# Kernel tuning notes

Measured on AMD Instinct MI355X. Metric: run time of the kernel, lower is better.

## Reference

```python
import jax, jax.numpy as jnp
import numpy as np

NUM_HEADS = 16
HEAD_DIM = 64


def setup_inputs() -> dict:
    key = jax.random.key(0)
    k1, k2, k3 = jax.random.split(key, 3)
    B, N, D = 4, 2048, NUM_HEADS * HEAD_DIM
    q = jax.random.normal(k1, (B, N, D), dtype=jnp.float32)
    k = jax.random.normal(k2, (B, N, D), dtype=jnp.float32)
    v = jax.random.normal(k3, (B, N, D), dtype=jnp.float32)
    # causal mask: True where attention is allowed
    attn_mask = jnp.tril(jnp.ones((N, N), dtype=bool))
    return {"q": q, "k": k, "v": v, "attn_mask": attn_mask}


def reference(q, k, v, attn_mask):
    B, N, D = q.shape
    H, Hd = NUM_HEADS, HEAD_DIM
    # [B, N, H*Hd] -> [B, H, N, Hd]
    qh = q.reshape(B, N, H, Hd).transpose(0, 2, 1, 3)
    kh = k.reshape(B, N, H, Hd).transpose(0, 2, 1, 3)
    vh = v.reshape(B, N, H, Hd).transpose(0, 2, 1, 3)
    scale = 1.0 / jnp.sqrt(jnp.asarray(Hd, dtype=q.dtype))
    scores = jnp.einsum('bhqd,bhkd->bhqk', qh, kh) * scale  # [B,H,N,N]
    scores = jnp.where(attn_mask[None, None, :, :], scores, -jnp.inf)
    probs = jax.nn.softmax(scores, axis=-1)
    y = jnp.einsum('bhqk,bhkd->bhqd', probs, vh)  # [B,H,N,Hd]
    return y.transpose(0, 2, 1, 3).reshape(B, N, H * Hd)
```

## Files before the change

### kernel.cpp

```cpp
#include <hip/hip_runtime.h>

#define RS 1024
#define SEQLEN 2048

typedef __fp16 f16;
typedef __attribute__((ext_vector_type(2))) __fp16 half2v;
typedef __attribute__((ext_vector_type(4))) __fp16 half4v;
typedef __attribute__((ext_vector_type(8))) __fp16 half8v;
typedef __attribute__((ext_vector_type(4))) float float4v;

__device__ __forceinline__ half8v pack8h(float4v a, float4v b) {
  union { half8v v; half2v h[4]; } u;
  u.h[0] = __builtin_amdgcn_cvt_pkrtz(a[0], a[1]);
  u.h[1] = __builtin_amdgcn_cvt_pkrtz(a[2], a[3]);
  u.h[2] = __builtin_amdgcn_cvt_pkrtz(b[0], b[1]);
  u.h[3] = __builtin_amdgcn_cvt_pkrtz(b[2], b[3]);
  return u.v;
}

template<bool DOMASK>
__device__ __forceinline__ void compute_tile(
    const f16* __restrict__ Klds, const f16* __restrict__ VB,
    const half8v (&aq)[2], float4v (&o)[4], float& lp,
    int quad, int lm, int wlm)
{
  float4v sfr[4];
  #pragma unroll
  for (int nb = 0; nb < 4; ++nb) sfr[nb] = (float4v){0.f, 0.f, 0.f, 0.f};

  __builtin_amdgcn_s_setprio(1);
  #pragma unroll
  for (int nb = 0; nb < 4; ++nb) {
    const int row = nb*16 + lm;
    #pragma unroll
    for (int s = 0; s < 2; ++s) {
      const half8v ak = *(const half8v*)&Klds[row*64 + (((s*4 + quad) ^ (lm & 7)) * 8)];
      sfr[nb] = __builtin_amdgcn_mfma_f32_16x16x32_f16(ak, aq[s], sfr[nb], 0, 0, 0);
    }
  }
  __builtin_amdgcn_s_setprio(0);

  half4v pa[4];
  float acc = 0.f;
  #pragma unroll
  for (int nb = 0; nb < 4; ++nb) {
    float p[4];
    #pragma unroll
    for (int r = 0; r < 4; ++r) {
      const int n = nb*16 + quad*4 + r;
      const float e = __builtin_amdgcn_exp2f(sfr[nb][r]);
      p[r] = (DOMASK && (n > wlm)) ? 0.f : e;
    }
    acc += (p[0] + p[1]) + (p[2] + p[3]);
    union { half4v v; half2v h[2]; } u;
    u.h[0] = __builtin_amdgcn_cvt_pkrtz(p[0], p[1]);
    u.h[1] = __builtin_amdgcn_cvt_pkrtz(p[2], p[3]);
    pa[nb] = u.v;
  }
  lp += acc;

  __builtin_amdgcn_s_setprio(1);
  #pragma unroll
  for (int nb = 0; nb < 4; ++nb) {
    const int kvq = nb*4 + quad;
    #pragma unroll
    for (int db = 0; db < 4; ++db) {
      const half4v vb = *(const half4v*)&VB[kvq*256 + (((db*16 + lm) ^ quad) * 4)];
      o[db] = __builtin_amdgcn_mfma_f32_16x16x16f16(pa[nb], vb, o[db], 0, 0, 0);
    }
  }
  __builtin_amdgcn_s_setprio(0);
}

__global__ __launch_bounds__(256, 4) void fa_fwd(
    const float* __restrict__ Qg, const float* __restrict__ Kg,
    const float* __restrict__ Vg, float* __restrict__ Og)
{
  __shared__ __align__(16) f16 Klds[2][64*64];
  __shared__ __align__(16) f16 VB[2][64*64];

  const int tid  = threadIdx.x;
  const int w    = tid >> 6;
  const int lane = tid & 63;
  const int quad = lane >> 4;
  const int lm   = lane & 15;
  const int wlm  = w*16 + lm;

  const int bid = blockIdx.x;
  const int bh  = bid & 63;
  const int t   = 31 - (bid >> 6);

  const size_t headoff = (size_t)(bh >> 4) * SEQLEN * RS + (size_t)(bh & 15) * 64;
  const float* Kb = Kg + headoff;
  const float* Vb = Vg + headoff;

  const float qs = 0.18033688011112042f;
  half8v aq[2];
  {
    const float* qp = Qg + headoff + (size_t)(t*64 + w*16 + lm) * RS + quad*8;
    aq[0] = pack8h(*(const float4v*)qp * qs,        *(const float4v*)(qp + 4) * qs);
    aq[1] = pack8h(*(const float4v*)(qp + 32) * qs, *(const float4v*)(qp + 36) * qs);
  }

  float4v o[4] = {};
  float lp = 0.f;

  const int krow = tid >> 3, kcb = tid & 7;
  const int rgrp = tid >> 4, dgrp = tid & 15;
  const int r3 = rgrp & 3;

  float4v pk[4], pv[4];
  auto loadKV = [&](int kv0) {
    const float* kp = Kb + (size_t)(kv0 + krow) * RS + kcb*8;
    pk[0] = *(const float4v*)kp;       pk[1] = *(const float4v*)(kp + 4);
    const float* kp2 = kp + (size_t)32 * RS;
    pk[2] = *(const float4v*)kp2;      pk[3] = *(const float4v*)(kp2 + 4);
    const float* vp = Vb + (size_t)(kv0 + rgrp*4) * RS + dgrp*4;
    pv[0] = *(const float4v*)vp;
    pv[1] = *(const float4v*)(vp + RS);
    pv[2] = *(const float4v*)(vp + 2*RS);
    pv[3] = *(const float4v*)(vp + 3*RS);
  };
  auto stageKV = [&](f16* Kd, f16* Vd) {
    *(half8v*)&Kd[krow*64 + ((kcb ^ (krow & 7)) * 8)] = pack8h(pk[0], pk[1]);
    const int row2 = krow + 32;
    *(half8v*)&Kd[row2*64 + ((kcb ^ (row2 & 7)) * 8)] = pack8h(pk[2], pk[3]);
    union { half8v v8[2]; half2v h[8]; } u;
    #pragma unroll
    for (int cp = 0; cp < 4; ++cp) {
      const int c = cp ^ r3;
      u.h[cp*2]     = __builtin_amdgcn_cvt_pkrtz(pv[0][c], pv[1][c]);
      u.h[cp*2 + 1] = __builtin_amdgcn_cvt_pkrtz(pv[2][c], pv[3][c]);
    }
    f16* dst = &Vd[rgrp*256 + dgrp*16];
    *(half8v*)dst       = u.v8[0];
    *(half8v*)(dst + 8) = u.v8[1];
  };

  loadKV(0);
  stageKV(Klds[0], VB[0]);
  if (t > 0) loadKV(64);
  __syncthreads();

  for (int j = 0; j <= t; ++j) {
    const int cur = j & 1;
    if (j < t) {
      stageKV(Klds[cur ^ 1], VB[cur ^ 1]);
      if (j + 1 < t) loadKV((j + 2) * 64);
    }
    if (j < t)
      compute_tile<false>(Klds[cur], VB[cur], aq, o, lp, quad, lm, wlm);
    else
      compute_tile<true >(Klds[cur], VB[cur], aq, o, lp, quad, lm, wlm);
    __syncthreads();
  }

  float l = lp;
  l += __shfl_xor(l, 16);
  l += __shfl_xor(l, 32);
  const float linv = 1.0f / l;
  #pragma unroll
  for (int r = 0; r < 4; ++r) {
    const float nrm = __shfl(linv, quad*4 + r);
    float* op = Og + headoff + (size_t)(t*64 + w*16 + quad*4 + r) * RS;
    #pragma unroll
    for (int db = 0; db < 4; ++db)
      op[db*16 + lm] = o[db][r] * nrm;
  }
}

extern "C" void kernel_launch(void* const* d_in, const int* in_sizes, int n_in,
                              void* d_out, int out_size, void* d_ws, size_t ws_size,
                              hipStream_t stream) {
  const float* q = (const float*)d_in[0];
  const float* k = (const float*)d_in[1];
  const float* v = (const float*)d_in[2];
  float* out = (float*)d_out;
  fa_fwd<<<dim3(32 * 64), dim3(256), 0, stream>>>(q, k, v, out);
}
```

Baseline: 200.4 us.

## Process 128 query rows per block with 8 waves sharing K/V tiles

Each block now covers 128 query rows with 512 threads (8 waves), so every K/V tile loaded into shared memory serves twice as many query rows and global K/V traffic is halved. The load work is split so the upper 256 threads fetch K and the lower 256 fetch V, which halves per-thread prefetch registers. The waves covering the first 64 rows skip the final diagonal tile while the other waves compute it, which leaves some waves idle on the last iteration. The grid shrinks from 2048 to 1024 blocks, reducing the number of blocks available to spread across CUs.

Result: faster. 181.4 us (-9.5%).

```diff
diff --git a/kernel.cpp b/kernel.cpp
--- a/kernel.cpp
+++ b/kernel.cpp
@@ -72,7 +72,7 @@
   __builtin_amdgcn_s_setprio(0);
 }
 
-__global__ __launch_bounds__(256, 4) void fa_fwd(
+__global__ __launch_bounds__(512, 4) void fa_fwd(
     const float* __restrict__ Qg, const float* __restrict__ Kg,
     const float* __restrict__ Vg, float* __restrict__ Og)
 {
@@ -84,11 +84,13 @@
   const int lane = tid & 63;
   const int quad = lane >> 4;
   const int lm   = lane & 15;
-  const int wlm  = w*16 + lm;
+  const int wlm  = (w & 3)*16 + lm;
 
   const int bid = blockIdx.x;
   const int bh  = bid & 63;
-  const int t   = 31 - (bid >> 6);
+  const int st  = 15 - (bid >> 6);
+  const int j1  = 2*st + 1;
+  const int j1w = 2*st + (w >> 2);
 
   const size_t headoff = (size_t)(bh >> 4) * SEQLEN * RS + (size_t)(bh & 15) * 64;
   const float* Kb = Kg + headoff;
@@ -97,7 +99,7 @@
   const float qs = 0.18033688011112042f;
   half8v aq[2];
   {
-    const float* qp = Qg + headoff + (size_t)(t*64 + w*16 + lm) * RS + quad*8;
+    const float* qp = Qg + headoff + (size_t)(st*128 + w*16 + lm) * RS + quad*8;
     aq[0] = pack8h(*(const float4v*)qp * qs,        *(const float4v*)(qp + 4) * qs);
     aq[1] = pack8h(*(const float4v*)(qp + 32) * qs, *(const float4v*)(qp + 36) * qs);
   }
@@ -105,53 +107,63 @@
   float4v o[4] = {};
   float lp = 0.f;
 
-  const int krow = tid >> 3, kcb = tid & 7;
-  const int rgrp = tid >> 4, dgrp = tid & 15;
+  const bool doK = (tid >= 256);
+  const int kr   = tid & 255;
+  const int krow = kr >> 3, kcb = kr & 7;
+  const int rgrp = kr >> 4, dgrp = kr & 15;
   const int r3 = rgrp & 3;
 
-  float4v pk[4], pv[4];
+  float4v pr[4];
   auto loadKV = [&](int kv0) {
-    const float* kp = Kb + (size_t)(kv0 + krow) * RS + kcb*8;
-    pk[0] = *(const float4v*)kp;       pk[1] = *(const float4v*)(kp + 4);
-    const float* kp2 = kp + (size_t)32 * RS;
-    pk[2] = *(const float4v*)kp2;      pk[3] = *(const float4v*)(kp2 + 4);
-    const float* vp = Vb + (size_t)(kv0 + rgrp*4) * RS + dgrp*4;
-    pv[0] = *(const float4v*)vp;
-    pv[1] = *(const float4v*)(vp + RS);
-    pv[2] = *(const float4v*)(vp + 2*RS);
-    pv[3] = *(const float4v*)(vp + 3*RS);
+    if (doK) {
+      const float* kp = Kb + (size_t)(kv0 + krow) * RS + kcb*8;
+      pr[0] = *(const float4v*)kp;       pr[1] = *(const float4v*)(kp + 4);
+      const float* kp2 = kp + (size_t)32 * RS;
+      pr[2] = *(const float4v*)kp2;      pr[3] = *(const float4v*)(kp2 + 4);
+    } else {
+      const float* vp = Vb + (size_t)(kv0 + rgrp*4) * RS + dgrp*4;
+      pr[0] = *(const float4v*)vp;
+      pr[1] = *(const float4v*)(vp + RS);
+      pr[2] = *(const float4v*)(vp + 2*RS);
+      pr[3] = *(const float4v*)(vp + 3*RS);
+    }
   };
   auto stageKV = [&](f16* Kd, f16* Vd) {
-    *(half8v*)&Kd[krow*64 + ((kcb ^ (krow & 7)) * 8)] = pack8h(pk[0], pk[1]);
-    const int row2 = krow + 32;
-    *(half8v*)&Kd[row2*64 + ((kcb ^ (row2 & 7)) * 8)] = pack8h(pk[2], pk[3]);
-    union { half8v v8[2]; half2v h[8]; } u;
-    #pragma unroll
-    for (int cp = 0; cp < 4; ++cp) {
-      const int c = cp ^ r3;
-      u.h[cp*2]     = __builtin_amdgcn_cvt_pkrtz(pv[0][c], pv[1][c]);
-      u.h[cp*2 + 1] = __builtin_amdgcn_cvt_pkrtz(pv[2][c], pv[3][c]);
+    if (doK) {
+      *(half8v*)&Kd[krow*64 + ((kcb ^ (krow & 7)) * 8)] = pack8h(pr[0], pr[1]);
+      const int row2 = krow + 32;
+      *(half8v*)&Kd[row2*64 + ((kcb ^ (row2 & 7)) * 8)] = pack8h(pr[2], pr[3]);
+    } else {
+      union { half8v v8[2]; half2v h[8]; } u;
+      #pragma unroll
+      for (int cp = 0; cp < 4; ++cp) {
+        const int c = cp ^ r3;
+        u.h[cp*2]     = __builtin_amdgcn_cvt_pkrtz(pr[0][c], pr[1][c]);
+        u.h[cp*2 + 1] = __builtin_amdgcn_cvt_pkrtz(pr[2][c], pr[3][c]);
+      }
+      f16* dst = &Vd[rgrp*256 + dgrp*16];
+      *(half8v*)dst       = u.v8[0];
+      *(half8v*)(dst + 8) = u.v8[1];
     }
-    f16* dst = &Vd[rgrp*256 + dgrp*16];
-    *(half8v*)dst       = u.v8[0];
-    *(half8v*)(dst + 8) = u.v8[1];
   };
 
   loadKV(0);
   stageKV(Klds[0], VB[0]);
-  if (t > 0) loadKV(64);
+  loadKV(64);
   __syncthreads();
 
-  for (int j = 0; j <= t; ++j) {
+  for (int j = 0; j <= j1; ++j) {
     const int cur = j & 1;
-    if (j < t) {
+    if (j < j1) {
       stageKV(Klds[cur ^ 1], VB[cur ^ 1]);
-      if (j + 1 < t) loadKV((j + 2) * 64);
+      if (j + 1 < j1) loadKV((j + 2) * 64);
     }
-    if (j < t)
-      compute_tile<false>(Klds[cur], VB[cur], aq, o, lp, quad, lm, wlm);
-    else
-      compute_tile<true >(Klds[cur], VB[cur], aq, o, lp, quad, lm, wlm);
+    if (j <= j1w) {
+      if (j < j1w)
+        compute_tile<false>(Klds[cur], VB[cur], aq, o, lp, quad, lm, wlm);
+      else
+        compute_tile<true >(Klds[cur], VB[cur], aq, o, lp, quad, lm, wlm);
+    }
     __syncthreads();
   }
 
@@ -162,7 +174,7 @@
   #pragma unroll
   for (int r = 0; r < 4; ++r) {
     const float nrm = __shfl(linv, quad*4 + r);
-    float* op = Og + headoff + (size_t)(t*64 + w*16 + quad*4 + r) * RS;
+    float* op = Og + headoff + (size_t)(st*128 + w*16 + quad*4 + r) * RS;
     #pragma unroll
     for (int db = 0; db < 4; ++db)
       op[db*16 + lm] = o[db][r] * nrm;
@@ -176,5 +188,5 @@
   const float* k = (const float*)d_in[1];
   const float* v = (const float*)d_in[2];
   float* out = (float*)d_out;
-  fa_fwd<<<dim3(32 * 64), dim3(256), 0, stream>>>(q, k, v, out);
+  fa_fwd<<<dim3(16 * 64), dim3(512), 0, stream>>>(q, k, v, out);
 }
```
